# Kernel tuning notes

Measured on AMD Instinct MI355X. Metric: run time of the kernel, lower is better.

The kernel has to match this reference:

```python
import jax, jax.numpy as jnp
import numpy as np

N_FEATURES = 256
D_TOKEN = 512
BATCH = 2048
EPS = 1e-5  # torch LayerNorm default


def setup_inputs() -> dict:
    key = jax.random.key(0)
    k1, k2, k3, k4 = jax.random.split(key, 4)
    values = jax.random.normal(k1, (BATCH, N_FEATURES), dtype=jnp.float32)
    masks = jax.random.uniform(k2, (BATCH, N_FEATURES), dtype=jnp.float32)
    # per-feature Linear(2, d_token): weights stacked as (n_features, 2, d_token)
    bound = 1.0 / np.sqrt(2.0)  # torch Linear init bound for in_features=2
    W = jax.random.uniform(k3, (N_FEATURES, 2, D_TOKEN), dtype=jnp.float32,
                           minval=-bound, maxval=bound)
    b = jax.random.uniform(k4, (N_FEATURES, D_TOKEN), dtype=jnp.float32,
                           minval=-bound, maxval=bound)
    gamma = jnp.ones((D_TOKEN,), dtype=jnp.float32)
    beta = jnp.zeros((D_TOKEN,), dtype=jnp.float32)
    return {"values": values, "masks": masks, "W": W, "b": b,
            "gamma": gamma, "beta": beta}


def reference(values, masks, W, b, gamma, beta):
    # (B, F, 2): stack value and mask per feature (matches torch.stack dim=1 per feature)
    x = jnp.stack([values, masks], axis=-1)
    # batched tiny GEMM over features: one fused einsum instead of F separate Linears
    tokens = jnp.einsum('bfi,fid->bfd', x, W) + b  # (B, F, D)
    # LayerNorm over last dim
    mu = jnp.mean(tokens, axis=-1, keepdims=True)
    var = jnp.var(tokens, axis=-1, keepdims=True)
    normed = (tokens - mu) * jax.lax.rsqrt(var + EPS)
    return normed * gamma + beta
```

## Files before the change

kernel.cpp:

```cpp
#include <hip/hip_runtime.h>

#define BATCH  2048
#define NFEAT  256
#define DTOK   512
#define EPS    1e-5f
#define BCHUNK 16

typedef float fx4 __attribute__((ext_vector_type(4)));

__global__ __launch_bounds__(256) void FeatureTokenizer_kernel(
    const float* __restrict__ values,
    const float* __restrict__ masks,
    const float* __restrict__ W,
    const float* __restrict__ bias,
    const float* __restrict__ gamma,
    const float* __restrict__ beta,
    float* __restrict__ out)
{
    const int lane = threadIdx.x & 63;
    const int wv   = threadIdx.x >> 6;
    const int bid  = blockIdx.x;
    const int fg   = bid & 63;
    const int bc   = bid >> 6;
    const int f    = fg * 4 + wv;
    const int b0   = bc * BCHUNK;

    const int dA = lane * 4;
    const int dB = dA + 256;

    const float* w0base = W + ((size_t)f * 2 + 0) * DTOK;
    const float* w1base = W + ((size_t)f * 2 + 1) * DTOK;
    const float* bbase  = bias + (size_t)f * DTOK;

    const fx4 w0a = *(const fx4*)(w0base + dA);
    const fx4 w0b = *(const fx4*)(w0base + dB);
    const fx4 w1a = *(const fx4*)(w1base + dA);
    const fx4 w1b = *(const fx4*)(w1base + dB);
    const fx4 ba  = *(const fx4*)(bbase  + dA);
    const fx4 bb  = *(const fx4*)(bbase  + dB);
    const fx4 ga  = *(const fx4*)(gamma + dA);
    const fx4 gb  = *(const fx4*)(gamma + dB);
    const fx4 ea  = *(const fx4*)(beta  + dA);
    const fx4 eb  = *(const fx4*)(beta  + dB);

    float vv = 0.0f, mm = 0.0f;
    if (lane < BCHUNK) {
        vv = values[(size_t)(b0 + lane) * NFEAT + f];
        mm = masks [(size_t)(b0 + lane) * NFEAT + f];
    }

    for (int i = 0; i < BCHUNK; ++i) {
        const float v = __shfl(vv, i, 64);
        const float m = __shfl(mm, i, 64);

        float t[8];
#pragma unroll
        for (int j = 0; j < 4; ++j) {
            t[j]     = fmaf(v, w0a[j], fmaf(m, w1a[j], ba[j]));
            t[j + 4] = fmaf(v, w0b[j], fmaf(m, w1b[j], bb[j]));
        }

        float s = 0.0f, ss = 0.0f;
#pragma unroll
        for (int j = 0; j < 8; ++j) {
            s  += t[j];
            ss += t[j] * t[j];
        }
#pragma unroll
        for (int off = 1; off < 64; off <<= 1) {
            s  += __shfl_xor(s,  off, 64);
            ss += __shfl_xor(ss, off, 64);
        }

        const float mu   = s * (1.0f / DTOK);
        const float var  = ss * (1.0f / DTOK) - mu * mu;
        const float rstd = rsqrtf(var + EPS);

        fx4 oA, oB;
#pragma unroll
        for (int j = 0; j < 4; ++j) {
            oA[j] = fmaf((t[j]     - mu) * rstd, ga[j], ea[j]);
            oB[j] = fmaf((t[j + 4] - mu) * rstd, gb[j], eb[j]);
        }

        float* orow = out + ((size_t)(b0 + i) * NFEAT + f) * DTOK;
        __builtin_nontemporal_store(oA, (fx4*)(orow + dA));
        __builtin_nontemporal_store(oB, (fx4*)(orow + dB));
    }
}

extern "C" void kernel_launch(void* const* d_in, const int* in_sizes, int n_in,
                              void* d_out, int out_size, void* d_ws, size_t ws_size,
                              hipStream_t stream) {
    const float* values = (const float*)d_in[0];
    const float* masks  = (const float*)d_in[1];
    const float* W      = (const float*)d_in[2];
    const float* bias   = (const float*)d_in[3];
    const float* gamma  = (const float*)d_in[4];
    const float* beta   = (const float*)d_in[5];
    float* out = (float*)d_out;

    const int blocks = 64 * (BATCH / BCHUNK);
    FeatureTokenizer_kernel<<<blocks, 256, 0, stream>>>(
        values, masks, W, bias, gamma, beta, out);
}
```

Baseline: 209.0 us.

## Precompute per-feature weight Gram moments to compute LayerNorm stats in closed form

Each token is linear in (value, mask), so its mean and second moment can be written from per-feature sums and pairwise dot products of the weight and bias vectors. The kernel now reduces these nine moments once per wave. Each batch row then gets its mean and variance from a few FMAs instead of a 6-step shuffle reduction. The values and masks loads are also changed from a lane load plus broadcast shuffle to direct per-row loads. This risks slightly different rounding in the variance.

```diff
diff --git a/kernel.cpp b/kernel.cpp
--- a/kernel.cpp
+++ b/kernel.cpp
@@ -43,44 +43,60 @@
     const fx4 ea  = *(const fx4*)(beta  + dA);
     const fx4 eb  = *(const fx4*)(beta  + dB);
 
-    float vv = 0.0f, mm = 0.0f;
-    if (lane < BCHUNK) {
-        vv = values[(size_t)(b0 + lane) * NFEAT + f];
-        mm = masks [(size_t)(b0 + lane) * NFEAT + f];
+    float a0 = 0, a1 = 0, a2 = 0;
+    float b00 = 0, b11 = 0, b22 = 0, b01 = 0, b02 = 0, b12 = 0;
+#pragma unroll
+    for (int j = 0; j < 4; ++j) {
+        const float u0 = w0a[j], u1 = w1a[j], ub = ba[j];
+        const float x0 = w0b[j], x1 = w1b[j], xb = bb[j];
+        a0 += u0 + x0;  a1 += u1 + x1;  a2 += ub + xb;
+        b00 = fmaf(u0, u0, fmaf(x0, x0, b00));
+        b11 = fmaf(u1, u1, fmaf(x1, x1, b11));
+        b22 = fmaf(ub, ub, fmaf(xb, xb, b22));
+        b01 = fmaf(u0, u1, fmaf(x0, x1, b01));
+        b02 = fmaf(u0, ub, fmaf(x0, xb, b02));
+        b12 = fmaf(u1, ub, fmaf(x1, xb, b12));
     }
 
+#pragma unroll
+    for (int off = 1; off < 64; off <<= 1) {
+        a0  += __shfl_xor(a0,  off, 64);
+        a1  += __shfl_xor(a1,  off, 64);
+        a2  += __shfl_xor(a2,  off, 64);
+        b00 += __shfl_xor(b00, off, 64);
+        b11 += __shfl_xor(b11, off, 64);
+        b22 += __shfl_xor(b22, off, 64);
+        b01 += __shfl_xor(b01, off, 64);
+        b02 += __shfl_xor(b02, off, 64);
+        b12 += __shfl_xor(b12, off, 64);
+    }
+
+    float vs[BCHUNK], ms[BCHUNK];
+#pragma unroll
     for (int i = 0; i < BCHUNK; ++i) {
-        const float v = __shfl(vv, i, 64);
-        const float m = __shfl(mm, i, 64);
+        vs[i] = values[(size_t)(b0 + i) * NFEAT + f];
+        ms[i] = masks [(size_t)(b0 + i) * NFEAT + f];
+    }
 
-        float t[8];
-#pragma unroll
-        for (int j = 0; j < 4; ++j) {
-            t[j]     = fmaf(v, w0a[j], fmaf(m, w1a[j], ba[j]));
-            t[j + 4] = fmaf(v, w0b[j], fmaf(m, w1b[j], bb[j]));
-        }
+#pragma unroll 4
+    for (int i = 0; i < BCHUNK; ++i) {
+        const float v = vs[i], m = ms[i];
 
-        float s = 0.0f, ss = 0.0f;
-#pragma unroll
-        for (int j = 0; j < 8; ++j) {
-            s  += t[j];
-            ss += t[j] * t[j];
-        }
-#pragma unroll
-        for (int off = 1; off < 64; off <<= 1) {
-            s  += __shfl_xor(s,  off, 64);
-            ss += __shfl_xor(ss, off, 64);
-        }
-
-        const float mu   = s * (1.0f / DTOK);
-        const float var  = ss * (1.0f / DTOK) - mu * mu;
+        const float S  = fmaf(v, a0, fmaf(m, a1, a2));
+        const float mu = S * (1.0f / DTOK);
+        const float E2 = fmaf(v * v, b00, fmaf(m * m, b11,
+                         fmaf(2.0f * v * m, b01,
+                         fmaf(2.0f * v, b02, fmaf(2.0f * m, b12, b22)))));
+        const float var  = E2 * (1.0f / DTOK) - mu * mu;
         const float rstd = rsqrtf(var + EPS);
 
         fx4 oA, oB;
 #pragma unroll
         for (int j = 0; j < 4; ++j) {
-            oA[j] = fmaf((t[j]     - mu) * rstd, ga[j], ea[j]);
-            oB[j] = fmaf((t[j + 4] - mu) * rstd, gb[j], eb[j]);
+            const float tA = fmaf(v, w0a[j], fmaf(m, w1a[j], ba[j]));
+            const float tB = fmaf(v, w0b[j], fmaf(m, w1b[j], bb[j]));
+            oA[j] = fmaf((tA - mu) * rstd, ga[j], ea[j]);
+            oB[j] = fmaf((tB - mu) * rstd, gb[j], eb[j]);
         }
 
         float* orow = out + ((size_t)(b0 + i) * NFEAT + f) * DTOK;
```

New measurement: 199.7 us (median of 2 runs). 4.4% less time.
